# Kernel tuning notes

Measured on AMD Instinct MI355X. Metric: run time of the kernel, lower is better.

The kernel has to match this reference:

```python
import jax, jax.numpy as jnp
import numpy as np

G, T, E = 20000, 2, 4        # n_genes, n_tech, n_expansion
U = G * T                    # independent tiny-linear units
N_ETH = 4                    # ethnicity cardinality (interaction index stride)
DNN_DIMS = [20038, 5009, 1252, 313, 78, 2]  # shrinkage_factor=4, min=64, final=2


def setup_inputs() -> dict:
    key = jax.random.key(0)
    ks = jax.random.split(key, 24)
    B = 512
    inp = {
        "expression": jax.random.normal(ks[0], (B, T, G), jnp.float32),
        "clinical_categorical": jax.random.randint(ks[1], (B, 3), 0, 4),
        "clinical_non_categorical": jax.random.normal(ks[2], (B, 2, 10), jnp.float32),
        # ParallelBellowsLayers params
        "bw1": 0.05 * jax.random.normal(ks[3], (U, E), jnp.float32),
        "bb1": 0.05 * jax.random.normal(ks[4], (U, E), jnp.float32),
        "bw2": 0.05 * jax.random.normal(ks[5], (U, E), jnp.float32),
        "bb2": 0.05 * jax.random.normal(ks[6], (U,), jnp.float32),
        # ParallelGeneLayers params
        "gw": 0.05 * jax.random.normal(ks[7], (G, T), jnp.float32),
        "gb": 0.05 * jax.random.normal(ks[8], (G,), jnp.float32),
        # embeddings
        "race_emb": 0.05 * jax.random.normal(ks[9], (10, 8), jnp.float32),
        "eth_emb": 0.05 * jax.random.normal(ks[10], (4, 4), jnp.float32),
        "inter_emb": 0.05 * jax.random.normal(ks[11], (40, 8), jnp.float32),
        "prot_emb": 0.05 * jax.random.normal(ks[12], (20, 8), jnp.float32),
        # ClinicalMissingMask params (n_variables=10)
        "mask_w": 0.05 * jax.random.normal(ks[13], (10, 2), jnp.float32),
        "mask_b": 0.05 * jax.random.normal(ks[14], (10,), jnp.float32),
    }
    for i in range(5):
        din, dout = DNN_DIMS[i], DNN_DIMS[i + 1]
        inp[f"dnn_w{i}"] = (jax.random.normal(ks[15 + i], (din, dout), jnp.float32)
                             / jnp.sqrt(jnp.float32(din)))
        inp[f"dnn_b{i}"] = jnp.zeros((dout,), jnp.float32)
    return inp


def _forward(expression, clinical_categorical, clinical_non_categorical,
             bw1, bb1, bw2, bb2, gw, gb,
             race_emb, eth_emb, inter_emb, prot_emb, mask_w, mask_b,
             dnn_w0, dnn_b0, dnn_w1, dnn_b1, dnn_w2, dnn_b2,
             dnn_w3, dnn_b3, dnn_w4, dnn_b4):
    B = expression.shape[0]
    # --- CombinedGeneModel ---
    # bellows: per-unit 1->E->1 linear; units are tech-major (view(B,T,G))
    xf = expression.reshape(B, U)                              # [B, U]
    h = jax.nn.relu(xf[:, :, None] * bw1[None] + bb1[None])    # [B, U, E]
    s = jax.nn.relu(jnp.einsum('bue,ue->bu', h, bw2) + bb2)    # [B, U]
    # per-gene combine over tech
    s3 = s.reshape(B, T, G)
    expr = jax.nn.relu(jnp.einsum('btg,gt->bg', s3, gw) + gb)  # [B, G]
    # --- ClinicalModel ---
    cc = clinical_categorical
    race = race_emb[cc[:, 0]]
    eth = eth_emb[cc[:, 1]]
    inter = inter_emb[cc[:, 0] * N_ETH + cc[:, 1]]
    prot = prot_emb[cc[:, 2]]
    nc = jax.nn.relu(jnp.einsum('bcv,vc->bv', clinical_non_categorical, mask_w)
                     + mask_b)                                 # [B, 10]
    clin = jnp.concatenate([race, eth, inter, prot, nc], axis=1)
    # --- ConnectedLayers (shrinking MLP) ---
    x = jnp.concatenate([expr, clin], axis=1)                  # [B, 20038]
    for w, b in [(dnn_w0, dnn_b0), (dnn_w1, dnn_b1),
                 (dnn_w2, dnn_b2), (dnn_w3, dnn_b3)]:
        x = jax.nn.relu(x @ w + b)
    return x @ dnn_w4 + dnn_b4                                 # [B, 2]


def reference(expression, clinical_categorical, clinical_non_categorical,
              bw1, bb1, bw2, bb2, gw, gb,
              race_emb, eth_emb, inter_emb, prot_emb, mask_w, mask_b,
              dnn_w0, dnn_b0, dnn_w1, dnn_b1, dnn_w2, dnn_b2,
              dnn_w3, dnn_b3, dnn_w4, dnn_b4):
    return _forward(expression, clinical_categorical, clinical_non_categorical,
                    bw1, bb1, bw2, bb2, gw, gb,
                    race_emb, eth_emb, inter_emb, prot_emb, mask_w, mask_b,
                    dnn_w0, dnn_b0, dnn_w1, dnn_b1, dnn_w2, dnn_b2,
                    dnn_w3, dnn_b3, dnn_w4, dnn_b4)
```

## Files before the change

kernel.cpp:

```cpp
#include <hip/hip_runtime.h>
#include <hip/hip_bf16.h>

typedef __attribute__((ext_vector_type(8))) short bf16x8;
typedef __attribute__((ext_vector_type(4))) float f32x4;
typedef __attribute__((ext_vector_type(4))) int   i32x4;
typedef __attribute__((ext_vector_type(4))) unsigned short u16x4;
typedef unsigned short u16;

#define G_ 20000
#define B_ 512

__device__ __forceinline__ u16 f2bf(float x) {
  __hip_bfloat16 h = __float2bfloat16(x);
  return __builtin_bit_cast(u16, h);
}
__device__ __forceinline__ float bf2f(u16 u) {
  unsigned int v = ((unsigned int)u) << 16;
  return __builtin_bit_cast(float, v);
}

__global__ void k_gene(const float* __restrict__ expr,
                       const float* __restrict__ bw1, const float* __restrict__ bb1,
                       const float* __restrict__ bw2, const float* __restrict__ bb2,
                       const float* __restrict__ gw,  const float* __restrict__ gb,
                       u16* __restrict__ Xt) {
  int g = blockIdx.x * 256 + threadIdx.x;
  if (g >= G_) return;
  int b0 = blockIdx.y * 32;

  f32x4 w1a = ((const f32x4*)bw1)[g];
  f32x4 w1b = ((const f32x4*)bw1)[G_ + g];
  f32x4 b1a = ((const f32x4*)bb1)[g];
  f32x4 b1b = ((const f32x4*)bb1)[G_ + g];
  f32x4 w2a = ((const f32x4*)bw2)[g];
  f32x4 w2b = ((const f32x4*)bw2)[G_ + g];
  float bb2a = bb2[g], bb2b = bb2[G_ + g];
  float gw0 = gw[g * 2], gw1 = gw[g * 2 + 1];
  float gbg = gb[g];

  u16* outp = Xt + (size_t)(g >> 5) * 16384 + (g & 31);

  #pragma unroll 4
  for (int b = b0; b < b0 + 32; ++b) {
    float x0 = expr[(size_t)(b * 2) * G_ + g];
    float x1 = expr[(size_t)(b * 2 + 1) * G_ + g];
    float h0 = fmaxf(x0 * w1a.x + b1a.x, 0.f);
    float h1 = fmaxf(x0 * w1a.y + b1a.y, 0.f);
    float h2 = fmaxf(x0 * w1a.z + b1a.z, 0.f);
    float h3 = fmaxf(x0 * w1a.w + b1a.w, 0.f);
    float s0 = fmaxf(h0 * w2a.x + h1 * w2a.y + h2 * w2a.z + h3 * w2a.w + bb2a, 0.f);
    float g0 = fmaxf(x1 * w1b.x + b1b.x, 0.f);
    float g1 = fmaxf(x1 * w1b.y + b1b.y, 0.f);
    float g2 = fmaxf(x1 * w1b.z + b1b.z, 0.f);
    float g3 = fmaxf(x1 * w1b.w + b1b.w, 0.f);
    float s1 = fmaxf(g0 * w2b.x + g1 * w2b.y + g2 * w2b.z + g3 * w2b.w + bb2b, 0.f);
    float e = fmaxf(s0 * gw0 + s1 * gw1 + gbg, 0.f);
    outp[(size_t)b * 32] = f2bf(e);
  }
}

__global__ void k_clin(const int* __restrict__ cc, const float* __restrict__ cnc,
                       const float* __restrict__ race, const float* __restrict__ eth,
                       const float* __restrict__ inter, const float* __restrict__ prot,
                       const float* __restrict__ mw, const float* __restrict__ mb,
                       u16* __restrict__ Xt) {
  int b = threadIdx.x;
  int c0 = cc[b * 3], c1 = cc[b * 3 + 1], c2 = cc[b * 3 + 2];
  float nc[10];
  #pragma unroll
  for (int v = 0; v < 10; ++v)
    nc[v] = fmaxf(cnc[b * 20 + v] * mw[v * 2] + cnc[b * 20 + 10 + v] * mw[v * 2 + 1] + mb[v], 0.f);

  u16* t0 = Xt + (size_t)625 * 16384 + b * 32;
  u16* t1 = Xt + (size_t)626 * 16384 + b * 32;
  #pragma unroll
  for (int c = 0; c < 32; ++c) {
    float v;
    if (c < 8)       v = race[c0 * 8 + c];
    else if (c < 12) v = eth[c1 * 4 + (c - 8)];
    else if (c < 20) v = inter[(c0 * 4 + c1) * 8 + (c - 12)];
    else if (c < 28) v = prot[c2 * 8 + (c - 20)];
    else             v = nc[c - 28];
    t0[c] = f2bf(v);
  }
  #pragma unroll
  for (int c = 0; c < 32; ++c) {
    int j = 32 + c;
    float v = (j < 38) ? nc[j - 28] : 0.f;
    t1[c] = f2bf(v);
  }
}

__global__ __launch_bounds__(512) void k_gemm(
    const u16* __restrict__ Xt, const float* __restrict__ W,
    float* __restrict__ part, int nSteps, int Kvalid, int Nvalid, int Npad) {
  __shared__ __align__(16) u16 Xs[512 * 40];
  __shared__ __align__(16) u16 Ws[128 * 40];

  const int tid = threadIdx.x;
  const int nt = blockIdx.x, split = blockIdx.y, S = gridDim.y;
  const int n0 = nt * 128;
  const int ks0 = (int)(((long)split * nSteps) / S);
  const int ks1 = (int)(((long)(split + 1) * nSteps) / S);

  const int lane = tid & 63, wave = tid >> 6;
  const int wr = wave >> 1, wc = wave & 1;
  const int l15 = lane & 15, l4 = lane >> 4;
  const int xn = tid & 127, kq = tid >> 7;

  f32x4 acc[8][4];
  #pragma unroll
  for (int i = 0; i < 8; ++i)
    #pragma unroll
    for (int j = 0; j < 4; ++j)
      #pragma unroll
      for (int r = 0; r < 4; ++r) acc[i][j][r] = 0.f;

  i32x4 xreg[4];
  float wreg[8];
  const int nW = n0 + xn;
  const bool nok = nW < Nvalid;

  auto LOAD = [&](int ks) {
    const i32x4* src = (const i32x4*)(Xt + (size_t)ks * 16384);
    #pragma unroll
    for (int p = 0; p < 4; ++p) xreg[p] = src[p * 512 + tid];
    long kb = (long)ks * 32 + kq * 8;
    #pragma unroll
    for (int i = 0; i < 8; ++i) {
      long k = kb + i;
      wreg[i] = (nok && k < (long)Kvalid) ? W[k * (size_t)Nvalid + nW] : 0.f;
    }
  };
  auto STORE = [&]() {
    #pragma unroll
    for (int p = 0; p < 4; ++p) {
      int chunk = p * 512 + tid;
      int row = chunk >> 2, c = chunk & 3;
      *(i32x4*)&Xs[row * 40 + c * 8] = xreg[p];
    }
    u16 h[8];
    #pragma unroll
    for (int i = 0; i < 8; ++i) h[i] = f2bf(wreg[i]);
    i32x4 pk;
    pk[0] = (int)h[0] | ((int)h[1] << 16);
    pk[1] = (int)h[2] | ((int)h[3] << 16);
    pk[2] = (int)h[4] | ((int)h[5] << 16);
    pk[3] = (int)h[6] | ((int)h[7] << 16);
    *(i32x4*)&Ws[xn * 40 + kq * 8] = pk;
  };

  LOAD(ks0);
  for (int ks = ks0; ks < ks1; ++ks) {
    __syncthreads();
    STORE();
    __syncthreads();
    if (ks + 1 < ks1) LOAD(ks + 1);

    bf16x8 af[8], bfr[4];
    #pragma unroll
    for (int mf = 0; mf < 8; ++mf)
      af[mf] = *(const bf16x8*)&Xs[(wr * 128 + mf * 16 + l15) * 40 + l4 * 8];
    #pragma unroll
    for (int nf = 0; nf < 4; ++nf)
      bfr[nf] = *(const bf16x8*)&Ws[(wc * 64 + nf * 16 + l15) * 40 + l4 * 8];
    #pragma unroll
    for (int mf = 0; mf < 8; ++mf)
      #pragma unroll
      for (int nf = 0; nf < 4; ++nf)
        acc[mf][nf] = __builtin_amdgcn_mfma_f32_16x16x32_bf16(af[mf], bfr[nf], acc[mf][nf], 0, 0, 0);
  }

  float* outp = part + (size_t)split * B_ * Npad;
  #pragma unroll
  for (int mf = 0; mf < 8; ++mf)
    #pragma unroll
    for (int nf = 0; nf < 4; ++nf) {
      int col = n0 + wc * 64 + nf * 16 + l15;
      int rb = wr * 128 + mf * 16 + l4 * 4;
      #pragma unroll
      for (int r = 0; r < 4; ++r)
        outp[(size_t)(rb + r) * Npad + col] = acc[mf][nf][r];
    }
}

__global__ void k_reduce(const float* __restrict__ part, const float* __restrict__ bias,
                         u16* __restrict__ Ht, int S, int Npad, int Nout, int Nvalid) {
  int idx = blockIdx.x * 256 + threadIdx.x;
  int perRow = Nout >> 2;
  if (idx >= B_ * perRow) return;
  int b = idx / perRow;
  int n = (idx - b * perRow) * 4;
  float v[4] = {0.f, 0.f, 0.f, 0.f};
  for (int s = 0; s < S; ++s) {
    const f32x4 p = *(const f32x4*)&part[(size_t)s * B_ * Npad + (size_t)b * Npad + n];
    #pragma unroll
    for (int r = 0; r < 4; ++r) v[r] += p[r];
  }
  u16x4 o;
  #pragma unroll
  for (int r = 0; r < 4; ++r) {
    float bi = (n + r < Nvalid) ? bias[n + r] : 0.f;
    o[r] = f2bf(fmaxf(v[r] + bi, 0.f));
  }
  *(u16x4*)&Ht[(size_t)(n >> 5) * 16384 + b * 32 + (n & 31)] = o;
}

__global__ void k_tail(const u16* __restrict__ H3t,
                       const float* __restrict__ W3, const float* __restrict__ b3,
                       const float* __restrict__ W4, const float* __restrict__ b4,
                       float* __restrict__ out) {
  __shared__ float h3[320];
  __shared__ float h4[80];
  int b = blockIdx.x, tid = threadIdx.x;
  for (int i = tid; i < 313; i += 128)
    h3[i] = bf2f(H3t[(size_t)(i >> 5) * 16384 + b * 32 + (i & 31)]);
  __syncthreads();
  if (tid < 78) {
    float a = b3[tid];
    for (int k = 0; k < 313; ++k) a += h3[k] * W3[k * 78 + tid];
    h4[tid] = fmaxf(a, 0.f);
  }
  __syncthreads();
  if (tid < 2) {
    float a = b4[tid];
    for (int k = 0; k < 78; ++k) a += h4[k] * W4[k * 2 + tid];
    out[b * 2 + tid] = a;
  }
}

extern "C" void kernel_launch(void* const* d_in, const int* in_sizes, int n_in,
                              void* d_out, int out_size, void* d_ws, size_t ws_size,
                              hipStream_t stream) {
  const float* expr = (const float*)d_in[0];
  const int*   cc   = (const int*)d_in[1];
  const float* cnc  = (const float*)d_in[2];
  const float* bw1  = (const float*)d_in[3];
  const float* bb1  = (const float*)d_in[4];
  const float* bw2  = (const float*)d_in[5];
  const float* bb2  = (const float*)d_in[6];
  const float* gw   = (const float*)d_in[7];
  const float* gb   = (const float*)d_in[8];
  const float* race = (const float*)d_in[9];
  const float* eth  = (const float*)d_in[10];
  const float* inter= (const float*)d_in[11];
  const float* prot = (const float*)d_in[12];
  const float* mw   = (const float*)d_in[13];
  const float* mb   = (const float*)d_in[14];
  const float* w0 = (const float*)d_in[15]; const float* b0 = (const float*)d_in[16];
  const float* w1 = (const float*)d_in[17]; const float* b1 = (const float*)d_in[18];
  const float* w2 = (const float*)d_in[19]; const float* b2 = (const float*)d_in[20];
  const float* w3 = (const float*)d_in[21]; const float* b3 = (const float*)d_in[22];
  const float* w4 = (const float*)d_in[23]; const float* b4 = (const float*)d_in[24];

  u16* Xt  = (u16*)d_ws;
  u16* H1t = Xt  + (size_t)627 * 16384;
  u16* H2t = H1t + (size_t)160 * 16384;
  u16* H3t = H2t + (size_t)40 * 16384;
  float* part = (float*)(H3t + (size_t)10 * 16384);

  k_gene<<<dim3(79, 16), 256, 0, stream>>>(expr, bw1, bb1, bw2, bb2, gw, gb, Xt);
  k_clin<<<1, 512, 0, stream>>>(cc, cnc, race, eth, inter, prot, mw, mb, Xt);

  k_gemm<<<dim3(40, 6), 512, 0, stream>>>(Xt, w0, part, 627, 20038, 5009, 5120);
  k_reduce<<<2560, 256, 0, stream>>>(part, b0, H1t, 6, 5120, 5120, 5009);

  k_gemm<<<dim3(10, 24), 512, 0, stream>>>(H1t, w1, part, 160, 5009, 1252, 1280);
  k_reduce<<<640, 256, 0, stream>>>(part, b1, H2t, 24, 1280, 1280, 1252);

  k_gemm<<<dim3(3, 40), 512, 0, stream>>>(H2t, w2, part, 40, 1252, 313, 384);
  k_reduce<<<160, 256, 0, stream>>>(part, b2, H3t, 40, 384, 320, 313);

  k_tail<<<512, 128, 0, stream>>>(H3t, w3, b3, w4, b4, (float*)d_out);
}
```

Baseline: 308.6 us.

## Widen GEMM K-slab to 64, double-buffer A in LDS with XOR swizzle

Changes the blocked activation layout from 32-wide to 64-wide K slabs across all producer and consumer kernels. The GEMM now double-buffers the A tile in LDS, uses an XOR swizzle instead of padding to avoid bank conflicts, and prefetches two slabs ahead with raw barriers. It also halves the number of synchronisations per K and cuts split-K counts for the later layers, which shrinks the reductions. The trade-off is more LDS and registers per block, and launch_bounds(512,2) may force register spills.

```diff
diff --git a/kernel.cpp b/kernel.cpp
--- a/kernel.cpp
+++ b/kernel.cpp
@@ -38,7 +38,7 @@
   float gw0 = gw[g * 2], gw1 = gw[g * 2 + 1];
   float gbg = gb[g];
 
-  u16* outp = Xt + (size_t)(g >> 5) * 16384 + (g & 31);
+  u16* outp = Xt + (size_t)(g >> 6) * 32768 + (g & 63);
 
   #pragma unroll 4
   for (int b = b0; b < b0 + 32; ++b) {
@@ -55,7 +55,7 @@
     float g3 = fmaxf(x1 * w1b.w + b1b.w, 0.f);
     float s1 = fmaxf(g0 * w2b.x + g1 * w2b.y + g2 * w2b.z + g3 * w2b.w + bb2b, 0.f);
     float e = fmaxf(s0 * gw0 + s1 * gw1 + gbg, 0.f);
-    outp[(size_t)b * 32] = f2bf(e);
+    outp[(size_t)b * 64] = f2bf(e);
   }
 }
 
@@ -71,104 +71,129 @@
   for (int v = 0; v < 10; ++v)
     nc[v] = fmaxf(cnc[b * 20 + v] * mw[v * 2] + cnc[b * 20 + 10 + v] * mw[v * 2 + 1] + mb[v], 0.f);
 
-  u16* t0 = Xt + (size_t)625 * 16384 + b * 32;
-  u16* t1 = Xt + (size_t)626 * 16384 + b * 32;
-  #pragma unroll
-  for (int c = 0; c < 32; ++c) {
+  #pragma unroll
+  for (int j = 0; j < 96; ++j) {
     float v;
-    if (c < 8)       v = race[c0 * 8 + c];
-    else if (c < 12) v = eth[c1 * 4 + (c - 8)];
-    else if (c < 20) v = inter[(c0 * 4 + c1) * 8 + (c - 12)];
-    else if (c < 28) v = prot[c2 * 8 + (c - 20)];
-    else             v = nc[c - 28];
-    t0[c] = f2bf(v);
-  }
-  #pragma unroll
-  for (int c = 0; c < 32; ++c) {
-    int j = 32 + c;
-    float v = (j < 38) ? nc[j - 28] : 0.f;
-    t1[c] = f2bf(v);
-  }
-}
-
-__global__ __launch_bounds__(512) void k_gemm(
+    if (j < 8)       v = race[c0 * 8 + j];
+    else if (j < 12) v = eth[c1 * 4 + (j - 8)];
+    else if (j < 20) v = inter[(c0 * 4 + c1) * 8 + (j - 12)];
+    else if (j < 28) v = prot[c2 * 8 + (j - 20)];
+    else if (j < 38) v = nc[j - 28];
+    else             v = 0.f;
+    int k = 20000 + j;
+    Xt[(size_t)(k >> 6) * 32768 + b * 64 + (k & 63)] = f2bf(v);
+  }
+}
+
+__global__ __launch_bounds__(512, 2) void k_gemm(
     const u16* __restrict__ Xt, const float* __restrict__ W,
-    float* __restrict__ part, int nSteps, int Kvalid, int Nvalid, int Npad) {
-  __shared__ __align__(16) u16 Xs[512 * 40];
-  __shared__ __align__(16) u16 Ws[128 * 40];
+    float* __restrict__ part, int nSlabs, int Kvalid, int Nvalid, int Npad) {
+  __shared__ __align__(16) u16 As[2][512 * 64];
+  __shared__ __align__(16) u16 Bs[128 * 64];
 
   const int tid = threadIdx.x;
   const int nt = blockIdx.x, split = blockIdx.y, S = gridDim.y;
   const int n0 = nt * 128;
-  const int ks0 = (int)(((long)split * nSteps) / S);
-  const int ks1 = (int)(((long)(split + 1) * nSteps) / S);
+  const int s0 = (int)(((long)split * nSlabs) / S);
+  const int s1 = (int)(((long)(split + 1) * nSlabs) / S);
+  const int sLast = s1 - 1;
 
   const int lane = tid & 63, wave = tid >> 6;
   const int wr = wave >> 1, wc = wave & 1;
   const int l15 = lane & 15, l4 = lane >> 4;
-  const int xn = tid & 127, kq = tid >> 7;
+
+  const int bn = tid & 127, bh = tid >> 7;
+  const int nW = n0 + bn;
+  const bool nok = nW < Nvalid;
 
   f32x4 acc[8][4];
   #pragma unroll
   for (int i = 0; i < 8; ++i)
     #pragma unroll
     for (int j = 0; j < 4; ++j)
+      acc[i][j] = f32x4{0.f, 0.f, 0.f, 0.f};
+
+  i32x4 areg[8];
+  float wreg[16];
+
+  auto ALOAD = [&](int s) {
+    const i32x4* src = (const i32x4*)(Xt + (size_t)s * 32768);
+    #pragma unroll
+    for (int i = 0; i < 8; ++i) areg[i] = src[i * 512 + tid];
+  };
+  auto WLOAD = [&](int s) {
+    int kb = s * 64 + bh * 16;
+    #pragma unroll
+    for (int j = 0; j < 16; ++j) {
+      int k = kb + j;
+      wreg[j] = (nok && k < Kvalid) ? W[(size_t)k * Nvalid + nW] : 0.f;
+    }
+  };
+  auto ASTORE = [&](int buf) {
+    #pragma unroll
+    for (int i = 0; i < 8; ++i) {
+      int lin = i * 512 + tid;
+      int m = lin >> 3, cch = lin & 7;
+      *(i32x4*)&As[buf][m * 64 + ((cch ^ (m & 7)) << 3)] = areg[i];
+    }
+  };
+  auto BSTORE = [&]() {
+    #pragma unroll
+    for (int h = 0; h < 2; ++h) {
+      i32x4 pk;
       #pragma unroll
-      for (int r = 0; r < 4; ++r) acc[i][j][r] = 0.f;
-
-  i32x4 xreg[4];
-  float wreg[8];
-  const int nW = n0 + xn;
-  const bool nok = nW < Nvalid;
-
-  auto LOAD = [&](int ks) {
-    const i32x4* src = (const i32x4*)(Xt + (size_t)ks * 16384);
-    #pragma unroll
-    for (int p = 0; p < 4; ++p) xreg[p] = src[p * 512 + tid];
-    long kb = (long)ks * 32 + kq * 8;
-    #pragma unroll
-    for (int i = 0; i < 8; ++i) {
-      long k = kb + i;
-      wreg[i] = (nok && k < (long)Kvalid) ? W[k * (size_t)Nvalid + nW] : 0.f;
-    }
-  };
-  auto STORE = [&]() {
-    #pragma unroll
-    for (int p = 0; p < 4; ++p) {
-      int chunk = p * 512 + tid;
-      int row = chunk >> 2, c = chunk & 3;
-      *(i32x4*)&Xs[row * 40 + c * 8] = xreg[p];
-    }
-    u16 h[8];
-    #pragma unroll
-    for (int i = 0; i < 8; ++i) h[i] = f2bf(wreg[i]);
-    i32x4 pk;
-    pk[0] = (int)h[0] | ((int)h[1] << 16);
-    pk[1] = (int)h[2] | ((int)h[3] << 16);
-    pk[2] = (int)h[4] | ((int)h[5] << 16);
-    pk[3] = (int)h[6] | ((int)h[7] << 16);
-    *(i32x4*)&Ws[xn * 40 + kq * 8] = pk;
-  };
-
-  LOAD(ks0);
-  for (int ks = ks0; ks < ks1; ++ks) {
-    __syncthreads();
-    STORE();
-    __syncthreads();
-    if (ks + 1 < ks1) LOAD(ks + 1);
-
-    bf16x8 af[8], bfr[4];
-    #pragma unroll
-    for (int mf = 0; mf < 8; ++mf)
-      af[mf] = *(const bf16x8*)&Xs[(wr * 128 + mf * 16 + l15) * 40 + l4 * 8];
-    #pragma unroll
-    for (int nf = 0; nf < 4; ++nf)
-      bfr[nf] = *(const bf16x8*)&Ws[(wc * 64 + nf * 16 + l15) * 40 + l4 * 8];
-    #pragma unroll
-    for (int mf = 0; mf < 8; ++mf)
+      for (int q = 0; q < 4; ++q) {
+        u16 lo = f2bf(wreg[h * 8 + q * 2]);
+        u16 hi = f2bf(wreg[h * 8 + q * 2 + 1]);
+        pk[q] = (int)(unsigned)lo | ((int)(unsigned)hi << 16);
+      }
+      int cch = bh * 2 + h;
+      *(i32x4*)&Bs[bn * 64 + ((cch ^ (bn & 7)) << 3)] = pk;
+    }
+  };
+  auto COMPUTE = [&](int buf) {
+    #pragma unroll
+    for (int kk = 0; kk < 2; ++kk) {
+      bf16x8 bfr[4];
       #pragma unroll
-      for (int nf = 0; nf < 4; ++nf)
-        acc[mf][nf] = __builtin_amdgcn_mfma_f32_16x16x32_bf16(af[mf], bfr[nf], acc[mf][nf], 0, 0, 0);
+      for (int nf = 0; nf < 4; ++nf) {
+        int n = wc * 64 + nf * 16 + l15;
+        int cch = kk * 4 + l4;
+        bfr[nf] = *(const bf16x8*)&Bs[n * 64 + ((cch ^ (n & 7)) << 3)];
+      }
+      #pragma unroll
+      for (int mf = 0; mf < 8; ++mf) {
+        int m = wr * 128 + mf * 16 + l15;
+        int cch = kk * 4 + l4;
+        bf16x8 af = *(const bf16x8*)&As[buf][m * 64 + ((cch ^ (m & 7)) << 3)];
+        #pragma unroll
+        for (int nf = 0; nf < 4; ++nf)
+          acc[mf][nf] = __builtin_amdgcn_mfma_f32_16x16x32_bf16(af, bfr[nf], acc[mf][nf], 0, 0, 0);
+      }
+    }
+  };
+
+  WLOAD(s0); ALOAD(s0);
+  ASTORE(0); BSTORE();
+  {
+    int sn = (s0 + 1 > sLast) ? sLast : s0 + 1;
+    ALOAD(sn); WLOAD(sn);
+  }
+  asm volatile("s_waitcnt lgkmcnt(0)" ::: "memory");
+  __builtin_amdgcn_s_barrier();
+
+  int c = 0;
+  for (int s = s0; s < s1; ++s) {
+    int sp = (s + 2 > sLast) ? sLast : s + 2;
+    ASTORE(c ^ 1);
+    ALOAD(sp);
+    asm volatile("s_waitcnt lgkmcnt(0)" ::: "memory");
+    __builtin_amdgcn_s_barrier();
+    COMPUTE(c);
+    __builtin_amdgcn_s_barrier();
+    BSTORE();
+    WLOAD(sp);
+    c ^= 1;
   }
 
   float* outp = part + (size_t)split * B_ * Npad;
@@ -203,7 +228,7 @@
     float bi = (n + r < Nvalid) ? bias[n + r] : 0.f;
     o[r] = f2bf(fmaxf(v[r] + bi, 0.f));
   }
-  *(u16x4*)&Ht[(size_t)(n >> 5) * 16384 + b * 32 + (n & 31)] = o;
+  *(u16x4*)&Ht[(size_t)(n >> 6) * 32768 + b * 64 + (n & 63)] = o;
 }
 
 __global__ void k_tail(const u16* __restrict__ H3t,
@@ -214,7 +239,7 @@
   __shared__ float h4[80];
   int b = blockIdx.x, tid = threadIdx.x;
   for (int i = tid; i < 313; i += 128)
-    h3[i] = bf2f(H3t[(size_t)(i >> 5) * 16384 + b * 32 + (i & 31)]);
+    h3[i] = bf2f(H3t[(size_t)(i >> 6) * 32768 + b * 64 + (i & 63)]);
   __syncthreads();
   if (tid < 78) {
     float a = b3[tid];
@@ -254,22 +279,22 @@
   const float* w4 = (const float*)d_in[23]; const float* b4 = (const float*)d_in[24];
 
   u16* Xt  = (u16*)d_ws;
-  u16* H1t = Xt  + (size_t)627 * 16384;
-  u16* H2t = H1t + (size_t)160 * 16384;
-  u16* H3t = H2t + (size_t)40 * 16384;
-  float* part = (float*)(H3t + (size_t)10 * 16384);
+  u16* H1t = Xt  + (size_t)314 * 32768;
+  u16* H2t = H1t + (size_t)80 * 32768;
+  u16* H3t = H2t + (size_t)20 * 32768;
+  float* part = (float*)(H3t + (size_t)5 * 32768);
 
   k_gene<<<dim3(79, 16), 256, 0, stream>>>(expr, bw1, bb1, bw2, bb2, gw, gb, Xt);
   k_clin<<<1, 512, 0, stream>>>(cc, cnc, race, eth, inter, prot, mw, mb, Xt);
 
-  k_gemm<<<dim3(40, 6), 512, 0, stream>>>(Xt, w0, part, 627, 20038, 5009, 5120);
+  k_gemm<<<dim3(40, 6), 512, 0, stream>>>(Xt, w0, part, 314, 20038, 5009, 5120);
   k_reduce<<<2560, 256, 0, stream>>>(part, b0, H1t, 6, 5120, 5120, 5009);
 
-  k_gemm<<<dim3(10, 24), 512, 0, stream>>>(H1t, w1, part, 160, 5009, 1252, 1280);
-  k_reduce<<<640, 256, 0, stream>>>(part, b1, H2t, 24, 1280, 1280, 1252);
-
-  k_gemm<<<dim3(3, 40), 512, 0, stream>>>(H2t, w2, part, 40, 1252, 313, 384);
-  k_reduce<<<160, 256, 0, stream>>>(part, b2, H3t, 40, 384, 320, 313);
+  k_gemm<<<dim3(10, 12), 512, 0, stream>>>(H1t, w1, part, 80, 5009, 1252, 1280);
+  k_reduce<<<640, 256, 0, stream>>>(part, b1, H2t, 12, 1280, 1280, 1252);
+
+  k_gemm<<<dim3(3, 5), 512, 0, stream>>>(H2t, w2, part, 20, 1252, 313, 384);
+  k_reduce<<<160, 256, 0, stream>>>(part, b2, H3t, 5, 384, 320, 313);
 
   k_tail<<<512, 128, 0, stream>>>(H3t, w3, b3, w4, b4, (float*)d_out);
 }
```

New measurement: 323.5 us. 1.05x slower.
